# Kernel tuning notes

Measured on AMD Instinct MI355X. Metric: run time of the kernel, lower is better.

## Reference

```python
import jax, jax.numpy as jnp
import numpy as np

C = 1.0                 # Poincare ball curvature
PROJ_EPS = 1e-5         # boundary epsilon for projection
ACOSH_EPS = 1e-7        # numerical floor for arccosh argument


def setup_inputs() -> dict:
    key = jax.random.key(0)
    k1, k2 = jax.random.split(key)
    num_tokens, embed_dim = 30522, 64
    batch, seq = 4, 1024
    token_ids = jax.random.randint(k1, (batch, seq), 0, num_tokens, dtype=jnp.int64)
    weight = jax.random.normal(k2, (num_tokens, embed_dim), dtype=jnp.float32) * 0.05
    scale = jnp.asarray(0.5, dtype=jnp.float32)
    return {"token_ids": token_ids, "weight": weight, "scale": scale}


def _poincare_bias(token_ids, weight, scale):
    ids = jnp.clip(token_ids, 0, weight.shape[0] - 1)
    emb = weight[ids]                                   # (b, s, d)
    # project onto the Poincare ball: clip norm to (1 - eps) / sqrt(c)
    sqc = jnp.sqrt(C)
    max_norm = (1.0 - PROJ_EPS) / sqc
    norm = jnp.linalg.norm(emb, axis=-1, keepdims=True)
    emb = jnp.where(norm > max_norm, emb * (max_norm / jnp.maximum(norm, 1e-12)), emb)
    # pairwise hyperbolic distance via arccosh form (== Mobius-add/artanh form):
    # d(x,y) = (1/sqrt(c)) * arccosh(1 + 2c||x-y||^2 / ((1-c||x||^2)(1-c||y||^2)))
    x2 = jnp.sum(emb * emb, axis=-1)                    # (b, s)
    gram = jnp.einsum("bid,bjd->bij", emb, emb)        # (b, s, s)
    sqdist = jnp.maximum(x2[:, :, None] + x2[:, None, :] - 2.0 * gram, 0.0)
    denom = (1.0 - C * x2)[:, :, None] * (1.0 - C * x2)[:, None, :]
    arg = 1.0 + 2.0 * C * sqdist / denom
    dist = jnp.arccosh(jnp.maximum(arg, 1.0 + ACOSH_EPS)) / sqc
    return scale * -dist                                # (b, s, s)


def reference(token_ids, weight, scale):
    return _poincare_bias(token_ids, weight, scale)
```

## Files before the change

### kernel.cpp

```cpp
#include <hip/hip_runtime.h>
#include <hip/hip_bf16.h>

typedef __attribute__((ext_vector_type(8))) short bf16x8;
typedef __attribute__((ext_vector_type(4))) float f32x4;

#define EMB_DIM 64

__global__ __launch_bounds__(256) void gather_project_kernel(
    const int* __restrict__ ids, const float* __restrict__ weight,
    __hip_bfloat16* __restrict__ emb, float* __restrict__ x2,
    int n_tokens_total, int vocab)
{
    int token = blockIdx.x * 4 + (threadIdx.x >> 6);
    int lane  = threadIdx.x & 63;
    if (token >= n_tokens_total) return;

    int id = ids[token];
    id = min(max(id, 0), vocab - 1);

    float w = weight[(size_t)id * EMB_DIM + lane];

    float s = w * w;
    #pragma unroll
    for (int off = 32; off >= 1; off >>= 1) s += __shfl_xor(s, off);
    float nrm = sqrtf(s);
    const float max_norm = 0.99999f;
    if (nrm > max_norm) w *= max_norm / fmaxf(nrm, 1e-12f);

    __hip_bfloat16 h = __float2bfloat16(w);
    float hf = __bfloat162float(h);
    emb[(size_t)token * EMB_DIM + lane] = h;

    float s2 = hf * hf;
    #pragma unroll
    for (int off = 32; off >= 1; off >>= 1) s2 += __shfl_xor(s2, off);
    if (lane == 0) x2[token] = s2;
}

__global__ __launch_bounds__(256) void pair_bias_kernel(
    const __hip_bfloat16* __restrict__ emb, const float* __restrict__ x2,
    const float* __restrict__ scale_p, float* __restrict__ out, int S)
{
    const int b  = blockIdx.z;
    const int i0 = blockIdx.y * 32 + ((threadIdx.x >> 7) << 4);
    const int j0 = blockIdx.x * 32 + (((threadIdx.x >> 6) & 1) << 4);
    const int lane = threadIdx.x & 63;
    const int r = lane & 15;
    const int q = lane >> 4;

    const short* E  = (const short*)emb + (size_t)b * S * EMB_DIM;
    const short* Ea = E + (i0 + r) * EMB_DIM + q * 8;
    const short* Eb = E + (j0 + r) * EMB_DIM + q * 8;

    bf16x8 a0 = *(const bf16x8*)(Ea);
    bf16x8 a1 = *(const bf16x8*)(Ea + 32);
    bf16x8 b0 = *(const bf16x8*)(Eb);
    bf16x8 b1 = *(const bf16x8*)(Eb + 32);

    f32x4 acc = {0.f, 0.f, 0.f, 0.f};
    acc = __builtin_amdgcn_mfma_f32_16x16x32_bf16(a0, b0, acc, 0, 0, 0);
    acc = __builtin_amdgcn_mfma_f32_16x16x32_bf16(a1, b1, acc, 0, 0, 0);

    const float* x2B = x2 + (size_t)b * S;
    float xj   = x2B[j0 + r];
    f32x4 xi4  = *(const f32x4*)(x2B + i0 + q * 4);
    float scale = scale_p[0];

    float* O = out + ((size_t)b * S + i0 + q * 4) * S + j0 + r;

    #pragma unroll
    for (int t = 0; t < 4; ++t) {
        float g  = acc[t];
        float xi = xi4[t];
        float sq  = fmaxf(xi + xj - 2.f * g, 0.f);
        float den = (1.f - xi) * (1.f - xj);
        float u = fmaxf(2.f * sq / den, 1.1920929e-7f);
        float dist = logf(1.f + u + sqrtf(u * (u + 2.f)));
        O[t * S] = -scale * dist;
    }
}

extern "C" void kernel_launch(void* const* d_in, const int* in_sizes, int n_in,
                              void* d_out, int out_size, void* d_ws, size_t ws_size,
                              hipStream_t stream) {
    const int*   ids     = (const int*)d_in[0];
    const float* weight  = (const float*)d_in[1];
    const float* scale_p = (const float*)d_in[2];
    float*       out     = (float*)d_out;

    const int n_tok = in_sizes[0];
    const int vocab = in_sizes[1] / EMB_DIM;
    const int S     = out_size / n_tok;
    const int B     = n_tok / S;

    __hip_bfloat16* emb = (__hip_bfloat16*)d_ws;
    float* x2 = (float*)((char*)d_ws + (size_t)n_tok * EMB_DIM * sizeof(__hip_bfloat16));

    gather_project_kernel<<<(n_tok + 3) / 4, 256, 0, stream>>>(
        ids, weight, emb, x2, n_tok, vocab);

    dim3 grid(S / 32, S / 32, B);
    pair_bias_kernel<<<grid, 256, 0, stream>>>(emb, x2, scale_p, out, S);
}
```

Measured before the change: 77.63 us.

## Use 32x32 MFMA tiles per wave and fast hardware math intrinsics

Each wave now computes a 32x32 output tile with four 32x32x16 bf16 MFMAs instead of a 16x16 tile with two 16x16x32 MFMAs, and blocks cover 64x64 tiles, so the grid shrinks by four. This raises the output produced per embedding load and cuts block launch overhead. The epilogue replaces division, sqrtf and logf with the amdgcn rcp, sqrt and log2 intrinsics, trading accuracy for fewer instructions. The output is memory-write bound, so the effect depends on store coalescing: each lane row now writes 32 contiguous floats.

```diff
diff --git a/kernel.cpp b/kernel.cpp
--- a/kernel.cpp
+++ b/kernel.cpp
@@ -1,8 +1,9 @@
 #include <hip/hip_runtime.h>
 #include <hip/hip_bf16.h>
 
-typedef __attribute__((ext_vector_type(8))) short bf16x8;
-typedef __attribute__((ext_vector_type(4))) float f32x4;
+typedef __attribute__((ext_vector_type(8)))  short bf16x8;
+typedef __attribute__((ext_vector_type(4)))  float f32x4;
+typedef __attribute__((ext_vector_type(16))) float f32x16;
 
 #define EMB_DIM 64
 
@@ -41,42 +42,47 @@
     const __hip_bfloat16* __restrict__ emb, const float* __restrict__ x2,
     const float* __restrict__ scale_p, float* __restrict__ out, int S)
 {
-    const int b  = blockIdx.z;
-    const int i0 = blockIdx.y * 32 + ((threadIdx.x >> 7) << 4);
-    const int j0 = blockIdx.x * 32 + (((threadIdx.x >> 6) & 1) << 4);
+    const int b    = blockIdx.z;
+    const int wid  = threadIdx.x >> 6;
     const int lane = threadIdx.x & 63;
-    const int r = lane & 15;
-    const int q = lane >> 4;
+    const int i0   = blockIdx.y * 64 + (wid >> 1) * 32;
+    const int j0   = blockIdx.x * 64 + (wid & 1) * 32;
+    const int m    = lane & 31;
+    const int h    = lane >> 5;
 
     const short* E  = (const short*)emb + (size_t)b * S * EMB_DIM;
-    const short* Ea = E + (i0 + r) * EMB_DIM + q * 8;
-    const short* Eb = E + (j0 + r) * EMB_DIM + q * 8;
+    const short* Ea = E + (i0 + m) * EMB_DIM + h * 8;
+    const short* Eb = E + (j0 + m) * EMB_DIM + h * 8;
 
-    bf16x8 a0 = *(const bf16x8*)(Ea);
-    bf16x8 a1 = *(const bf16x8*)(Ea + 32);
-    bf16x8 b0 = *(const bf16x8*)(Eb);
-    bf16x8 b1 = *(const bf16x8*)(Eb + 32);
-
-    f32x4 acc = {0.f, 0.f, 0.f, 0.f};
-    acc = __builtin_amdgcn_mfma_f32_16x16x32_bf16(a0, b0, acc, 0, 0, 0);
-    acc = __builtin_amdgcn_mfma_f32_16x16x32_bf16(a1, b1, acc, 0, 0, 0);
+    f32x16 acc = {};
+    #pragma unroll
+    for (int kb = 0; kb < 4; ++kb) {
+        bf16x8 av = *(const bf16x8*)(Ea + kb * 16);
+        bf16x8 bv = *(const bf16x8*)(Eb + kb * 16);
+        acc = __builtin_amdgcn_mfma_f32_32x32x16_bf16(av, bv, acc, 0, 0, 0);
+    }
 
     const float* x2B = x2 + (size_t)b * S;
-    float xj   = x2B[j0 + r];
-    f32x4 xi4  = *(const f32x4*)(x2B + i0 + q * 4);
-    float scale = scale_p[0];
+    const float  xj    = x2B[j0 + m];
+    const float  scale = scale_p[0];
+    const float  omxj  = 1.f - xj;
 
-    float* O = out + ((size_t)b * S + i0 + q * 4) * S + j0 + r;
+    float* O = out + ((size_t)b * S + i0 + 4 * h) * S + j0 + m;
 
     #pragma unroll
-    for (int t = 0; t < 4; ++t) {
-        float g  = acc[t];
-        float xi = xi4[t];
-        float sq  = fmaxf(xi + xj - 2.f * g, 0.f);
-        float den = (1.f - xi) * (1.f - xj);
-        float u = fmaxf(2.f * sq / den, 1.1920929e-7f);
-        float dist = logf(1.f + u + sqrtf(u * (u + 2.f)));
-        O[t * S] = -scale * dist;
+    for (int g = 0; g < 4; ++g) {
+        f32x4 xi4 = *(const f32x4*)(x2B + i0 + g * 8 + 4 * h);
+        #pragma unroll
+        for (int e = 0; e < 4; ++e) {
+            float gv = acc[g * 4 + e];
+            float xi = xi4[e];
+            float sq  = fmaxf(xi + xj - 2.f * gv, 0.f);
+            float den = (1.f - xi) * omxj;
+            float u = fmaxf(2.f * sq * __builtin_amdgcn_rcpf(den), 1.1920929e-7f);
+            float w = 1.f + u + __builtin_amdgcn_sqrtf(u * (u + 2.f));
+            float dist = 0.69314718056f * __builtin_amdgcn_logf(w);
+            O[(size_t)(g * 8 + e) * S] = -scale * dist;
+        }
     }
 }
 
@@ -99,6 +105,6 @@
     gather_project_kernel<<<(n_tok + 3) / 4, 256, 0, stream>>>(
         ids, weight, emb, x2, n_tok, vocab);
 
-    dim3 grid(S / 32, S / 32, B);
+    dim3 grid(S / 64, S / 64, B);
     pair_bias_kernel<<<grid, 256, 0, stream>>>(emb, x2, scale_p, out, S);
 }
```

Result: faster. 74.30 us (-4.3%).
